# Performance work log

Hardware: AMD Instinct MI355X
Metric: run time of the kernel (lower is better)

The kernel has to match this reference:

```python
import jax, jax.numpy as jnp
import numpy as np

D_K = 64  # hard-coded in the original module
NEG = -1e9


def setup_inputs() -> dict:
    key = jax.random.key(0)
    kq, kk, kv, km = jax.random.split(key, 4)
    B, H, S, D = 2, 16, 2048, D_K
    Q = jax.random.normal(kq, (B, H, S, D), dtype=jnp.float32)
    K = jax.random.normal(kk, (B, H, S, D), dtype=jnp.float32)
    V = jax.random.normal(kv, (B, H, S, D), dtype=jnp.float32)
    attn_mask = jax.random.randint(km, (B, H, S, S), 0, 2).astype(jnp.bool_)
    return {"Q": Q, "K": K, "V": V, "attn_mask": attn_mask}


def reference(Q, K, V, attn_mask):
    # scores: [B, H, S, S]
    scores = jnp.einsum("bhqd,bhkd->bhqk", Q, K) / np.sqrt(D_K).astype(np.float32)
    scores = jnp.where(attn_mask, NEG, scores)
    attn = jax.nn.softmax(scores, axis=-1)
    context = jnp.einsum("bhqk,bhkd->bhqd", attn, V)
    return (context, attn)
```

## Files before the change

### kernel.cpp

```cpp
#include <hip/hip_runtime.h>
#include <stdint.h>


#define SEQ 2048
#define DK 64
#define NQT (SEQ / 16)
#define NBH 32

typedef unsigned int uint_t;
typedef unsigned long long u64;
typedef __attribute__((ext_vector_type(4))) float f32x4;
typedef __attribute__((ext_vector_type(8))) __bf16 bf16x8;
typedef __attribute__((ext_vector_type(8))) unsigned short ushort8_t;

#define SMEM_TOTAL 78208

__device__ __forceinline__ unsigned short f2bf(float f) {
  union { float f; unsigned int u; } v; v.f = f;
  unsigned int r = v.u + 0x7fffu + ((v.u >> 16) & 1u);
  return (unsigned short)(r >> 16);
}
__device__ __forceinline__ float bf2f(unsigned short b) {
  union { unsigned int u; float f; } v; v.u = ((unsigned int)b) << 16;
  return v.f;
}
__device__ __forceinline__ bf16x8 pack8(const float4& a, const float4& b) {
  union { unsigned short u[8]; bf16x8 v; } r;
  r.u[0] = f2bf(a.x); r.u[1] = f2bf(a.y); r.u[2] = f2bf(a.z); r.u[3] = f2bf(a.w);
  r.u[4] = f2bf(b.x); r.u[5] = f2bf(b.y); r.u[6] = f2bf(b.z); r.u[7] = f2bf(b.w);
  return r.v;
}

__global__ void detect_mode(const uint_t* __restrict__ m, int* __restrict__ flag) {
  __shared__ uint_t red[256];
  uint_t acc = 0;
  for (int i = threadIdx.x; i < 16384; i += 256) acc |= m[i];
  red[threadIdx.x] = acc;
  __syncthreads();
  for (int s = 128; s > 0; s >>= 1) {
    if ((int)threadIdx.x < s) red[threadIdx.x] |= red[threadIdx.x + s];
    __syncthreads();
  }
  if (threadIdx.x == 0) flag[0] = (red[0] > 1u) ? 1 : 0;
}

__global__ void __launch_bounds__(256, 2)
attn_fused(const float* __restrict__ Qg, const float* __restrict__ Kg,
           const float* __restrict__ Vg, const void* __restrict__ maskg,
           float* __restrict__ ctxg, float* __restrict__ attng,
           const int* __restrict__ modeflag) {
  extern __shared__ char smem[];
  unsigned short* v_lds = (unsigned short*)(smem + 65536);
  u64* mbits = (u64*)(smem + 73984);
  float* rowsum = (float*)(smem + 78080);
  float* invs = (float*)(smem + 78144);

  const int tid = threadIdx.x;
  const int lane = tid & 63;
  const int wave = tid >> 6;
  const int l15 = lane & 15;
  const int g = lane >> 4;

  const int qt = blockIdx.x;
  const int bh = blockIdx.y;
  const int qbase = qt * 16;
  const size_t bhSS = (size_t)bh * SEQ * SEQ;

  const float* Qb = Qg + ((size_t)bh * SEQ + qbase) * DK;
  const float* Kb = Kg + (size_t)bh * SEQ * DK;
  const float* Vb = Vg + (size_t)bh * SEQ * DK;
  float* attnb = attng + bhSS + (size_t)qbase * SEQ;
  float* ctxb = ctxg + ((size_t)bh * SEQ + qbase) * DK;

  const int byteMode = modeflag ? modeflag[0] : 0;

  if (tid < 16) rowsum[tid] = 0.0f;

  {
    const unsigned char* mb8 = (const unsigned char*)maskg;
    const uint_t* mb32 = (const uint_t*)maskg;
    for (int qi = 0; qi < 4; ++qi) {
      int q = wave * 4 + qi;
      size_t roff = bhSS + (size_t)(qbase + q) * SEQ;
      #pragma unroll
      for (int i = 0; i < 8; ++i) {
        uint_t m0, m1, m2, m3;
        if (byteMode) {
          uint_t v = *(const uint_t*)(mb8 + roff + i * 256 + lane * 4);
          m0 = v & 0xffu; m1 = v & 0xff00u; m2 = v & 0xff0000u; m3 = v & 0xff000000u;
        } else {
          uint4 v = *(const uint4*)(mb32 + roff + i * 256 + lane * 4);
          m0 = v.x; m1 = v.y; m2 = v.z; m3 = v.w;
        }
        u64 b0 = __ballot(m0 != 0u);
        u64 b1 = __ballot(m1 != 0u);
        u64 b2 = __ballot(m2 != 0u);
        u64 b3 = __ballot(m3 != 0u);
        if (lane == 0) {
          u64* w = &mbits[q * 32 + i * 4];
          w[0] = b0; w[1] = b1; w[2] = b2; w[3] = b3;
        }
      }
    }
  }

  const float* qrow = Qb + (size_t)l15 * DK + g * 8;
  float4 qa0 = *(const float4*)(qrow + 0);
  float4 qa1 = *(const float4*)(qrow + 4);
  float4 qb0 = *(const float4*)(qrow + 32);
  float4 qb1 = *(const float4*)(qrow + 36);
  bf16x8 aF0 = pack8(qa0, qa1);
  bf16x8 aF1 = pack8(qb0, qb1);

  __syncthreads();

  float rs0 = 0.f, rs1 = 0.f, rs2 = 0.f, rs3 = 0.f;
  const int kw = wave * 512;
  u64 mb0 = 0, mb1 = 0, mb2 = 0, mb3 = 0;
  #pragma unroll 4
  for (int t = 0; t < 32; ++t) {
    int k0 = kw + t * 16;
    const float* krow = Kb + (size_t)(k0 + l15) * DK + g * 8;
    float4 ka0 = *(const float4*)(krow + 0);
    float4 ka1 = *(const float4*)(krow + 4);
    float4 kb0 = *(const float4*)(krow + 32);
    float4 kb1 = *(const float4*)(krow + 36);
    bf16x8 bF0 = pack8(ka0, ka1);
    bf16x8 bF1 = pack8(kb0, kb1);
    f32x4 acc = {0.f, 0.f, 0.f, 0.f};
    acc = __builtin_amdgcn_mfma_f32_16x16x32_bf16(aF0, bF0, acc, 0, 0, 0);
    acc = __builtin_amdgcn_mfma_f32_16x16x32_bf16(aF1, bF1, acc, 0, 0, 0);

    if ((t & 15) == 0) {
      int widx = ((k0 >> 8) << 2) + (l15 & 3);
      mb0 = mbits[(g * 4 + 0) * 32 + widx];
      mb1 = mbits[(g * 4 + 1) * 32 + widx];
      mb2 = mbits[(g * 4 + 2) * 32 + widx];
      mb3 = mbits[(g * 4 + 3) * 32 + widx];
    }
    int shift = ((k0 >> 2) & 63) + (l15 >> 2);
    int kidx = k0 + l15;
    float p0 = ((mb0 >> shift) & 1) ? 0.f : __expf(acc[0] * 0.125f);
    float p1 = ((mb1 >> shift) & 1) ? 0.f : __expf(acc[1] * 0.125f);
    float p2 = ((mb2 >> shift) & 1) ? 0.f : __expf(acc[2] * 0.125f);
    float p3 = ((mb3 >> shift) & 1) ? 0.f : __expf(acc[3] * 0.125f);
    rs0 += p0; rs1 += p1; rs2 += p2; rs3 += p3;
    int q0 = g * 4;
    *(unsigned short*)(smem + (((q0 + 0) * 4096 + kidx * 2) ^ (((q0 + 0) & 7) << 4))) = f2bf(p0);
    *(unsigned short*)(smem + (((q0 + 1) * 4096 + kidx * 2) ^ (((q0 + 1) & 7) << 4))) = f2bf(p1);
    *(unsigned short*)(smem + (((q0 + 2) * 4096 + kidx * 2) ^ (((q0 + 2) & 7) << 4))) = f2bf(p2);
    *(unsigned short*)(smem + (((q0 + 3) * 4096 + kidx * 2) ^ (((q0 + 3) & 7) << 4))) = f2bf(p3);
  }

  rs0 += __shfl_xor(rs0, 1); rs0 += __shfl_xor(rs0, 2); rs0 += __shfl_xor(rs0, 4); rs0 += __shfl_xor(rs0, 8);
  rs1 += __shfl_xor(rs1, 1); rs1 += __shfl_xor(rs1, 2); rs1 += __shfl_xor(rs1, 4); rs1 += __shfl_xor(rs1, 8);
  rs2 += __shfl_xor(rs2, 1); rs2 += __shfl_xor(rs2, 2); rs2 += __shfl_xor(rs2, 4); rs2 += __shfl_xor(rs2, 8);
  rs3 += __shfl_xor(rs3, 1); rs3 += __shfl_xor(rs3, 2); rs3 += __shfl_xor(rs3, 4); rs3 += __shfl_xor(rs3, 8);
  if (l15 == 0) {
    atomicAdd(&rowsum[g * 4 + 0], rs0);
    atomicAdd(&rowsum[g * 4 + 1], rs1);
    atomicAdd(&rowsum[g * 4 + 2], rs2);
    atomicAdd(&rowsum[g * 4 + 3], rs3);
  }
  __syncthreads();
  if (tid < 16) invs[tid] = 1.0f / rowsum[tid];
  __syncthreads();

  for (int qi = 0; qi < 4; ++qi) {
    int q = wave * 4 + qi;
    float iq = invs[q];
    float* arow = attnb + (size_t)q * SEQ;
    #pragma unroll
    for (int i = 0; i < 4; ++i) {
      int k = i * 512 + lane * 8;
      int boff = (q * 4096 + k * 2) ^ ((q & 7) << 4);
      ushort8_t pv = *(ushort8_t*)(smem + boff);
      float4 o0, o1;
      o0.x = bf2f(pv[0]) * iq; o0.y = bf2f(pv[1]) * iq;
      o0.z = bf2f(pv[2]) * iq; o0.w = bf2f(pv[3]) * iq;
      o1.x = bf2f(pv[4]) * iq; o1.y = bf2f(pv[5]) * iq;
      o1.z = bf2f(pv[6]) * iq; o1.w = bf2f(pv[7]) * iq;
      *(float4*)(arow + k) = o0;
      *(float4*)(arow + k + 4) = o1;
    }
  }

  f32x4 cacc = {0.f, 0.f, 0.f, 0.f};
  for (int ck = 0; ck < 32; ++ck) {
    __syncthreads();
    #pragma unroll
    for (int s2 = 0; s2 < 4; ++s2) {
      int row = (tid >> 4) + s2 * 16;
      int c4 = (tid & 15) * 4;
      float4 v = *(const float4*)(Vb + (size_t)(ck * 64 + row) * DK + c4);
      uint_t lo = (uint_t)f2bf(v.x) | ((uint_t)f2bf(v.y) << 16);
      uint_t hi = (uint_t)f2bf(v.z) | ((uint_t)f2bf(v.w) << 16);
      *(uint_t*)(&v_lds[row * 66 + c4]) = lo;
      *(uint_t*)(&v_lds[row * 66 + c4 + 2]) = hi;
    }
    __syncthreads();
    #pragma unroll
    for (int c = 0; c < 2; ++c) {
      int boff = (l15 * 4096 + (ck * 64 + c * 32 + g * 8) * 2) ^ ((l15 & 7) << 4);
      ushort8_t pa = *(ushort8_t*)(smem + boff);
      union { ushort8_t u; bf16x8 v; } au; au.u = pa;
      union { unsigned short u[8]; bf16x8 v; } bu;
      int vbase = (c * 32 + g * 8) * 66 + wave * 16 + l15;
      #pragma unroll
      for (int j = 0; j < 8; ++j) bu.u[j] = v_lds[vbase + j * 66];
      cacc = __builtin_amdgcn_mfma_f32_16x16x32_bf16(au.v, bu.v, cacc, 0, 0, 0);
    }
  }
  #pragma unroll
  for (int r = 0; r < 4; ++r) {
    int q = g * 4 + r;
    ctxb[(size_t)q * DK + wave * 16 + l15] = cacc[r] * invs[q];
  }
}

extern "C" void kernel_launch(void* const* d_in, const int* in_sizes, int n_in,
                              void* d_out, int out_size, void* d_ws, size_t ws_size,
                              hipStream_t stream) {
  const float* Q = (const float*)d_in[0];
  const float* K = (const float*)d_in[1];
  const float* V = (const float*)d_in[2];
  const void* mask = d_in[3];
  float* ctx = (float*)d_out;
  float* attn = ctx + (size_t)2 * 16 * 2048 * 64;

  int* flag = (ws_size >= sizeof(int)) ? (int*)d_ws : nullptr;
  if (flag) {
    detect_mode<<<dim3(1), dim3(256), 0, stream>>>((const uint_t*)mask, flag);
  }

  (void)hipFuncSetAttribute((const void*)attn_fused,
                            hipFuncAttributeMaxDynamicSharedMemorySize, SMEM_TOTAL);
  dim3 grid(NQT, NBH);
  attn_fused<<<grid, dim3(256), SMEM_TOTAL, stream>>>(Q, K, V, mask, ctx, attn, flag);
}
```

Before: 1.399 ms.

## Pre-convert Q/K/V to bf16 MFMA fragments and keep probabilities in registers

```diff
diff --git a/kernel.cpp b/kernel.cpp
--- a/kernel.cpp
+++ b/kernel.cpp
@@ -4,25 +4,25 @@
 
 #define SEQ 2048
 #define DK 64
-#define NQT (SEQ / 16)
 #define NBH 32
 
 typedef unsigned int uint_t;
-typedef unsigned long long u64;
 typedef __attribute__((ext_vector_type(4))) float f32x4;
 typedef __attribute__((ext_vector_type(8))) __bf16 bf16x8;
-typedef __attribute__((ext_vector_type(8))) unsigned short ushort8_t;
-
-#define SMEM_TOTAL 78208
 
 __device__ __forceinline__ unsigned short f2bf(float f) {
   union { float f; unsigned int u; } v; v.f = f;
   unsigned int r = v.u + 0x7fffu + ((v.u >> 16) & 1u);
   return (unsigned short)(r >> 16);
 }
-__device__ __forceinline__ float bf2f(unsigned short b) {
-  union { unsigned int u; float f; } v; v.u = ((unsigned int)b) << 16;
-  return v.f;
+__device__ __forceinline__ uint_t pk2(float a, float b) {
+  return (uint_t)f2bf(a) | ((uint_t)f2bf(b) << 16);
+}
+__device__ __forceinline__ float lo2f(uint_t w) {
+  union { uint_t u; float f; } v; v.u = w << 16; return v.f;
+}
+__device__ __forceinline__ float hi2f(uint_t w) {
+  union { uint_t u; float f; } v; v.u = w & 0xffff0000u; return v.f;
 }
 __device__ __forceinline__ bf16x8 pack8(const float4& a, const float4& b) {
   union { unsigned short u[8]; bf16x8 v; } r;
@@ -30,6 +30,7 @@
   r.u[4] = f2bf(b.x); r.u[5] = f2bf(b.y); r.u[6] = f2bf(b.z); r.u[7] = f2bf(b.w);
   return r.v;
 }
+union BU { uint_t w[4]; bf16x8 v; };
 
 __global__ void detect_mode(const uint_t* __restrict__ m, int* __restrict__ flag) {
   __shared__ uint_t red[256];
@@ -44,16 +45,50 @@
   if (threadIdx.x == 0) flag[0] = (red[0] > 1u) ? 1 : 0;
 }
 
-__global__ void __launch_bounds__(256, 2)
+__global__ void __launch_bounds__(256)
+convert_qk(const float* __restrict__ Kg, const float* __restrict__ Qg,
+           void* __restrict__ Ktv, void* __restrict__ Qtv) {
+  int wid = blockIdx.x * 4 + (threadIdx.x >> 6);
+  int lane = threadIdx.x & 63;
+  int l15 = lane & 15, g = lane >> 4;
+  int arr = wid >> 13;
+  int rem = wid & 8191;
+  int bh = rem >> 8;
+  int t = (rem >> 1) & 127;
+  int h = rem & 1;
+  const float* src = arr ? Qg : Kg;
+  bf16x8* dst = (bf16x8*)(arr ? Qtv : Ktv);
+  const float* row = src + ((size_t)bh * SEQ + t * 16 + l15) * DK + h * 32 + g * 8;
+  dst[((size_t)(bh * 128 + t) * 2 + h) * 64 + lane] =
+      pack8(*(const float4*)row, *(const float4*)(row + 4));
+}
+
+__global__ void __launch_bounds__(256)
+convert_v(const float* __restrict__ Vg, void* __restrict__ Vtv) {
+  int wid = blockIdx.x * 4 + (threadIdx.x >> 6);
+  int lane = threadIdx.x & 63;
+  int l15 = lane & 15, g = lane >> 4;
+  int dblk = wid & 3;
+  int s = (wid >> 2) & 63;
+  int bh = wid >> 8;
+  union { unsigned short u[8]; bf16x8 v; } b;
+  const float* src = Vg + ((size_t)bh * SEQ + s * 32 + g * 8) * DK + dblk * 16 + l15;
+  #pragma unroll
+  for (int j = 0; j < 8; ++j) b.u[j] = f2bf(src[j * DK]);
+  ((bf16x8*)Vtv)[(size_t)wid * 64 + lane] = b.v;
+}
+
+template <bool PRE>
+__global__ void __launch_bounds__(256, 3)
 attn_fused(const float* __restrict__ Qg, const float* __restrict__ Kg,
            const float* __restrict__ Vg, const void* __restrict__ maskg,
            float* __restrict__ ctxg, float* __restrict__ attng,
-           const int* __restrict__ modeflag) {
-  extern __shared__ char smem[];
-  unsigned short* v_lds = (unsigned short*)(smem + 65536);
-  u64* mbits = (u64*)(smem + 73984);
-  float* rowsum = (float*)(smem + 78080);
-  float* invs = (float*)(smem + 78144);
+           const int* __restrict__ modeflag,
+           const void* __restrict__ Ktv, const void* __restrict__ Qtv,
+           const void* __restrict__ Vtv) {
+  __shared__ float ctx_lds[1024];
+  __shared__ float rowsum[16];
+  __shared__ float invs[16];
 
   const int tid = threadIdx.x;
   const int lane = tid & 63;
@@ -64,157 +99,148 @@
   const int qt = blockIdx.x;
   const int bh = blockIdx.y;
   const int qbase = qt * 16;
+  const int kw = wave * 512;
   const size_t bhSS = (size_t)bh * SEQ * SEQ;
 
-  const float* Qb = Qg + ((size_t)bh * SEQ + qbase) * DK;
+  for (int i = tid; i < 1024; i += 256) ctx_lds[i] = 0.f;
+  if (tid < 16) rowsum[tid] = 0.f;
+
+  const int byteMode = modeflag ? modeflag[0] : 0;
+
+  bf16x8 qB0, qB1;
+  if (PRE) {
+    const bf16x8* qtp = (const bf16x8*)Qtv + ((size_t)(bh * 128 + qt) * 2) * 64 + lane;
+    qB0 = qtp[0];
+    qB1 = qtp[64];
+  } else {
+    const float* qrow = Qg + ((size_t)bh * SEQ + qbase + l15) * DK + g * 8;
+    qB0 = pack8(*(const float4*)(qrow), *(const float4*)(qrow + 4));
+    qB1 = pack8(*(const float4*)(qrow + 32), *(const float4*)(qrow + 36));
+  }
+
+  uint_t p[64];
+  float rs = 0.f;
+  const size_t maskRow = bhSS + (size_t)(qbase + l15) * SEQ;
+  const uint_t* mask32 = (const uint_t*)maskg;
+  const unsigned char* mask8 = (const unsigned char*)maskg;
+  const bf16x8* ktp =
+      PRE ? ((const bf16x8*)Ktv + ((size_t)(bh * 128 + wave * 32) * 2) * 64 + lane) : nullptr;
   const float* Kb = Kg + (size_t)bh * SEQ * DK;
+
+  #pragma unroll
+  for (int t = 0; t < 32; ++t) {
+    bf16x8 kA0, kA1;
+    if (PRE) {
+      kA0 = ktp[t * 128];
+      kA1 = ktp[t * 128 + 64];
+    } else {
+      const float* krow = Kb + (size_t)(kw + t * 16 + l15) * DK + g * 8;
+      kA0 = pack8(*(const float4*)(krow), *(const float4*)(krow + 4));
+      kA1 = pack8(*(const float4*)(krow + 32), *(const float4*)(krow + 36));
+    }
+    int kcol = kw + t * 16 + 4 * g;
+    uint_t m0, m1, m2, m3;
+    if (byteMode) {
+      uint_t mv = *(const uint_t*)(mask8 + maskRow + kcol);
+      m0 = mv & 0xffu; m1 = mv & 0xff00u; m2 = mv & 0xff0000u; m3 = mv & 0xff000000u;
+    } else {
+      uint4 mv = *(const uint4*)(mask32 + maskRow + kcol);
+      m0 = mv.x; m1 = mv.y; m2 = mv.z; m3 = mv.w;
+    }
+    f32x4 acc = {0.f, 0.f, 0.f, 0.f};
+    acc = __builtin_amdgcn_mfma_f32_16x16x32_bf16(kA0, qB0, acc, 0, 0, 0);
+    acc = __builtin_amdgcn_mfma_f32_16x16x32_bf16(kA1, qB1, acc, 0, 0, 0);
+    float p0 = m0 ? 0.f : __expf(acc[0] * 0.125f);
+    float p1 = m1 ? 0.f : __expf(acc[1] * 0.125f);
+    float p2 = m2 ? 0.f : __expf(acc[2] * 0.125f);
+    float p3 = m3 ? 0.f : __expf(acc[3] * 0.125f);
+    rs += (p0 + p1) + (p2 + p3);
+    p[2 * t] = pk2(p0, p1);
+    p[2 * t + 1] = pk2(p2, p3);
+  }
+
+  rs += __shfl_xor(rs, 16);
+  rs += __shfl_xor(rs, 32);
+  __syncthreads();
+  if (g == 0) atomicAdd(&rowsum[l15], rs);
+  __syncthreads();
+  if (tid < 16) invs[tid] = 1.0f / rowsum[tid];
+  __syncthreads();
+  const float inv = invs[l15];
+
+  float* attnRow = attng + bhSS + (size_t)(qbase + l15) * SEQ + kw + 4 * g;
+  #pragma unroll
+  for (int t = 0; t < 32; ++t) {
+    float4 o;
+    o.x = lo2f(p[2 * t]) * inv;
+    o.y = hi2f(p[2 * t]) * inv;
+    o.z = lo2f(p[2 * t + 1]) * inv;
+    o.w = hi2f(p[2 * t + 1]) * inv;
+    *(float4*)(attnRow + t * 16) = o;
+  }
+
+  const int srcA = (2 * (g & 1)) * 16 + l15;
+  const int srcB = srcA + 16;
+  const bool hiT = (g >> 1) != 0;
+  f32x4 c0 = {0.f,0.f,0.f,0.f}, c1 = {0.f,0.f,0.f,0.f};
+  f32x4 c2 = {0.f,0.f,0.f,0.f}, c3 = {0.f,0.f,0.f,0.f};
+  const bf16x8* vtp =
+      PRE ? ((const bf16x8*)Vtv + ((size_t)(bh * 64 + wave * 16) * 4) * 64 + lane) : nullptr;
   const float* Vb = Vg + (size_t)bh * SEQ * DK;
-  float* attnb = attng + bhSS + (size_t)qbase * SEQ;
-  float* ctxb = ctxg + ((size_t)bh * SEQ + qbase) * DK;
-
-  const int byteMode = modeflag ? modeflag[0] : 0;
-
-  if (tid < 16) rowsum[tid] = 0.0f;
-
+
+  #pragma unroll
+  for (int s = 0; s < 16; ++s) {
+    uint_t plo0 = p[4 * s], phi0 = p[4 * s + 1];
+    uint_t plo1 = p[4 * s + 2], phi1 = p[4 * s + 3];
+    uint_t a0 = __shfl(plo0, srcA), b0 = __shfl(plo1, srcA);
+    uint_t a1 = __shfl(phi0, srcA), b1 = __shfl(phi1, srcA);
+    uint_t a2 = __shfl(plo0, srcB), b2 = __shfl(plo1, srcB);
+    uint_t a3 = __shfl(phi0, srcB), b3 = __shfl(phi1, srcB);
+    BU pa;
+    pa.w[0] = hiT ? b0 : a0;
+    pa.w[1] = hiT ? b1 : a1;
+    pa.w[2] = hiT ? b2 : a2;
+    pa.w[3] = hiT ? b3 : a3;
+    bf16x8 v0, v1, v2, v3;
+    if (PRE) {
+      v0 = vtp[s * 256 + 0];
+      v1 = vtp[s * 256 + 64];
+      v2 = vtp[s * 256 + 128];
+      v3 = vtp[s * 256 + 192];
+    } else {
+      union { unsigned short u[8]; bf16x8 v; } b[4];
+      int k0 = kw + 32 * s + g * 8;
+      #pragma unroll
+      for (int j = 0; j < 8; ++j) {
+        const float* vr = Vb + (size_t)(k0 + j) * DK + l15;
+        b[0].u[j] = f2bf(vr[0]);
+        b[1].u[j] = f2bf(vr[16]);
+        b[2].u[j] = f2bf(vr[32]);
+        b[3].u[j] = f2bf(vr[48]);
+      }
+      v0 = b[0].v; v1 = b[1].v; v2 = b[2].v; v3 = b[3].v;
+    }
+    c0 = __builtin_amdgcn_mfma_f32_16x16x32_bf16(pa.v, v0, c0, 0, 0, 0);
+    c1 = __builtin_amdgcn_mfma_f32_16x16x32_bf16(pa.v, v1, c1, 0, 0, 0);
+    c2 = __builtin_amdgcn_mfma_f32_16x16x32_bf16(pa.v, v2, c2, 0, 0, 0);
+    c3 = __builtin_amdgcn_mfma_f32_16x16x32_bf16(pa.v, v3, c3, 0, 0, 0);
+  }
+
+  #pragma unroll
+  for (int r = 0; r < 4; ++r) {
+    int q = 4 * g + r;
+    atomicAdd(&ctx_lds[q * 64 + l15], c0[r]);
+    atomicAdd(&ctx_lds[q * 64 + 16 + l15], c1[r]);
+    atomicAdd(&ctx_lds[q * 64 + 32 + l15], c2[r]);
+    atomicAdd(&ctx_lds[q * 64 + 48 + l15], c3[r]);
+  }
+  __syncthreads();
   {
-    const unsigned char* mb8 = (const unsigned char*)maskg;
-    const uint_t* mb32 = (const uint_t*)maskg;
-    for (int qi = 0; qi < 4; ++qi) {
-      int q = wave * 4 + qi;
-      size_t roff = bhSS + (size_t)(qbase + q) * SEQ;
-      #pragma unroll
-      for (int i = 0; i < 8; ++i) {
-        uint_t m0, m1, m2, m3;
-        if (byteMode) {
-          uint_t v = *(const uint_t*)(mb8 + roff + i * 256 + lane * 4);
-          m0 = v & 0xffu; m1 = v & 0xff00u; m2 = v & 0xff0000u; m3 = v & 0xff000000u;
-        } else {
-          uint4 v = *(const uint4*)(mb32 + roff + i * 256 + lane * 4);
-          m0 = v.x; m1 = v.y; m2 = v.z; m3 = v.w;
-        }
-        u64 b0 = __ballot(m0 != 0u);
-        u64 b1 = __ballot(m1 != 0u);
-        u64 b2 = __ballot(m2 != 0u);
-        u64 b3 = __ballot(m3 != 0u);
-        if (lane == 0) {
-          u64* w = &mbits[q * 32 + i * 4];
-          w[0] = b0; w[1] = b1; w[2] = b2; w[3] = b3;
-        }
-      }
-    }
-  }
-
-  const float* qrow = Qb + (size_t)l15 * DK + g * 8;
-  float4 qa0 = *(const float4*)(qrow + 0);
-  float4 qa1 = *(const float4*)(qrow + 4);
-  float4 qb0 = *(const float4*)(qrow + 32);
-  float4 qb1 = *(const float4*)(qrow + 36);
-  bf16x8 aF0 = pack8(qa0, qa1);
-  bf16x8 aF1 = pack8(qb0, qb1);
-
-  __syncthreads();
-
-  float rs0 = 0.f, rs1 = 0.f, rs2 = 0.f, rs3 = 0.f;
-  const int kw = wave * 512;
-  u64 mb0 = 0, mb1 = 0, mb2 = 0, mb3 = 0;
-  #pragma unroll 4
-  for (int t = 0; t < 32; ++t) {
-    int k0 = kw + t * 16;
-    const float* krow = Kb + (size_t)(k0 + l15) * DK + g * 8;
-    float4 ka0 = *(const float4*)(krow + 0);
-    float4 ka1 = *(const float4*)(krow + 4);
-    float4 kb0 = *(const float4*)(krow + 32);
-    float4 kb1 = *(const float4*)(krow + 36);
-    bf16x8 bF0 = pack8(ka0, ka1);
-    bf16x8 bF1 = pack8(kb0, kb1);
-    f32x4 acc = {0.f, 0.f, 0.f, 0.f};
-    acc = __builtin_amdgcn_mfma_f32_16x16x32_bf16(aF0, bF0, acc, 0, 0, 0);
-    acc = __builtin_amdgcn_mfma_f32_16x16x32_bf16(aF1, bF1, acc, 0, 0, 0);
-
-    if ((t & 15) == 0) {
-      int widx = ((k0 >> 8) << 2) + (l15 & 3);
-      mb0 = mbits[(g * 4 + 0) * 32 + widx];
-      mb1 = mbits[(g * 4 + 1) * 32 + widx];
-      mb2 = mbits[(g * 4 + 2) * 32 + widx];
-      mb3 = mbits[(g * 4 + 3) * 32 + widx];
-    }
-    int shift = ((k0 >> 2) & 63) + (l15 >> 2);
-    int kidx = k0 + l15;
-    float p0 = ((mb0 >> shift) & 1) ? 0.f : __expf(acc[0] * 0.125f);
-    float p1 = ((mb1 >> shift) & 1) ? 0.f : __expf(acc[1] * 0.125f);
-    float p2 = ((mb2 >> shift) & 1) ? 0.f : __expf(acc[2] * 0.125f);
-    float p3 = ((mb3 >> shift) & 1) ? 0.f : __expf(acc[3] * 0.125f);
-    rs0 += p0; rs1 += p1; rs2 += p2; rs3 += p3;
-    int q0 = g * 4;
-    *(unsigned short*)(smem + (((q0 + 0) * 4096 + kidx * 2) ^ (((q0 + 0) & 7) << 4))) = f2bf(p0);
-    *(unsigned short*)(smem + (((q0 + 1) * 4096 + kidx * 2) ^ (((q0 + 1) & 7) << 4))) = f2bf(p1);
-    *(unsigned short*)(smem + (((q0 + 2) * 4096 + kidx * 2) ^ (((q0 + 2) & 7) << 4))) = f2bf(p2);
-    *(unsigned short*)(smem + (((q0 + 3) * 4096 + kidx * 2) ^ (((q0 + 3) & 7) << 4))) = f2bf(p3);
-  }
-
-  rs0 += __shfl_xor(rs0, 1); rs0 += __shfl_xor(rs0, 2); rs0 += __shfl_xor(rs0, 4); rs0 += __shfl_xor(rs0, 8);
-  rs1 += __shfl_xor(rs1, 1); rs1 += __shfl_xor(rs1, 2); rs1 += __shfl_xor(rs1, 4); rs1 += __shfl_xor(rs1, 8);
-  rs2 += __shfl_xor(rs2, 1); rs2 += __shfl_xor(rs2, 2); rs2 += __shfl_xor(rs2, 4); rs2 += __shfl_xor(rs2, 8);
-  rs3 += __shfl_xor(rs3, 1); rs3 += __shfl_xor(rs3, 2); rs3 += __shfl_xor(rs3, 4); rs3 += __shfl_xor(rs3, 8);
-  if (l15 == 0) {
-    atomicAdd(&rowsum[g * 4 + 0], rs0);
-    atomicAdd(&rowsum[g * 4 + 1], rs1);
-    atomicAdd(&rowsum[g * 4 + 2], rs2);
-    atomicAdd(&rowsum[g * 4 + 3], rs3);
-  }
-  __syncthreads();
-  if (tid < 16) invs[tid] = 1.0f / rowsum[tid];
-  __syncthreads();
-
-  for (int qi = 0; qi < 4; ++qi) {
-    int q = wave * 4 + qi;
-    float iq = invs[q];
-    float* arow = attnb + (size_t)q * SEQ;
-    #pragma unroll
-    for (int i = 0; i < 4; ++i) {
-      int k = i * 512 + lane * 8;
-      int boff = (q * 4096 + k * 2) ^ ((q & 7) << 4);
-      ushort8_t pv = *(ushort8_t*)(smem + boff);
-      float4 o0, o1;
-      o0.x = bf2f(pv[0]) * iq; o0.y = bf2f(pv[1]) * iq;
-      o0.z = bf2f(pv[2]) * iq; o0.w = bf2f(pv[3]) * iq;
-      o1.x = bf2f(pv[4]) * iq; o1.y = bf2f(pv[5]) * iq;
-      o1.z = bf2f(pv[6]) * iq; o1.w = bf2f(pv[7]) * iq;
-      *(float4*)(arow + k) = o0;
-      *(float4*)(arow + k + 4) = o1;
-    }
-  }
-
-  f32x4 cacc = {0.f, 0.f, 0.f, 0.f};
-  for (int ck = 0; ck < 32; ++ck) {
-    __syncthreads();
-    #pragma unroll
-    for (int s2 = 0; s2 < 4; ++s2) {
-      int row = (tid >> 4) + s2 * 16;
-      int c4 = (tid & 15) * 4;
-      float4 v = *(const float4*)(Vb + (size_t)(ck * 64 + row) * DK + c4);
-      uint_t lo = (uint_t)f2bf(v.x) | ((uint_t)f2bf(v.y) << 16);
-      uint_t hi = (uint_t)f2bf(v.z) | ((uint_t)f2bf(v.w) << 16);
-      *(uint_t*)(&v_lds[row * 66 + c4]) = lo;
-      *(uint_t*)(&v_lds[row * 66 + c4 + 2]) = hi;
-    }
-    __syncthreads();
-    #pragma unroll
-    for (int c = 0; c < 2; ++c) {
-      int boff = (l15 * 4096 + (ck * 64 + c * 32 + g * 8) * 2) ^ ((l15 & 7) << 4);
-      ushort8_t pa = *(ushort8_t*)(smem + boff);
-      union { ushort8_t u; bf16x8 v; } au; au.u = pa;
-      union { unsigned short u[8]; bf16x8 v; } bu;
-      int vbase = (c * 32 + g * 8) * 66 + wave * 16 + l15;
-      #pragma unroll
-      for (int j = 0; j < 8; ++j) bu.u[j] = v_lds[vbase + j * 66];
-      cacc = __builtin_amdgcn_mfma_f32_16x16x32_bf16(au.v, bu.v, cacc, 0, 0, 0);
-    }
-  }
-  #pragma unroll
-  for (int r = 0; r < 4; ++r) {
-    int q = g * 4 + r;
-    ctxb[(size_t)q * DK + wave * 16 + l15] = cacc[r] * invs[q];
+    int e = tid * 4;
+    float iq = invs[e >> 6];
+    float4 v = *(const float4*)(ctx_lds + e);
+    float4 o = { v.x * iq, v.y * iq, v.z * iq, v.w * iq };
+    *(float4*)(ctxg + ((size_t)bh * SEQ + qbase) * DK + e) = o;
   }
 }
 
@@ -226,15 +252,26 @@
   const float* V = (const float*)d_in[2];
   const void* mask = d_in[3];
   float* ctx = (float*)d_out;
-  float* attn = ctx + (size_t)2 * 16 * 2048 * 64;
-
+  float* attn = ctx + (size_t)NBH * SEQ * DK;
+
+  const size_t FRAG = (size_t)NBH * 128 * 2 * 64 * 16;
+  const size_t WS_NEED = 1024 + 3 * FRAG;
+  bool pre = ws_size >= WS_NEED;
   int* flag = (ws_size >= sizeof(int)) ? (int*)d_ws : nullptr;
-  if (flag) {
-    detect_mode<<<dim3(1), dim3(256), 0, stream>>>((const uint_t*)mask, flag);
-  }
-
-  (void)hipFuncSetAttribute((const void*)attn_fused,
-                            hipFuncAttributeMaxDynamicSharedMemorySize, SMEM_TOTAL);
-  dim3 grid(NQT, NBH);
-  attn_fused<<<grid, dim3(256), SMEM_TOTAL, stream>>>(Q, K, V, mask, ctx, attn, flag);
-}
+  char* wsb = (char*)d_ws;
+  void* Kt = wsb + 1024;
+  void* Qt = wsb + 1024 + FRAG;
+  void* Vt = wsb + 1024 + 2 * FRAG;
+
+  if (flag) detect_mode<<<dim3(1), dim3(256), 0, stream>>>((const uint_t*)mask, flag);
+
+  dim3 grid(SEQ / 16, NBH);
+  if (pre) {
+    convert_qk<<<dim3(4096), dim3(256), 0, stream>>>(K, Q, Kt, Qt);
+    convert_v<<<dim3(2048), dim3(256), 0, stream>>>(V, Vt);
+    attn_fused<true><<<grid, dim3(256), 0, stream>>>(Q, K, V, mask, ctx, attn, flag, Kt, Qt, Vt);
+  } else {
+    attn_fused<false><<<grid, dim3(256), 0, stream>>>(Q, K, V, mask, ctx, attn, flag,
+                                                      nullptr, nullptr, nullptr);
+  }
+}
```

New measurement: 1.267 ms. 9.5% less time.
